# Kernel tuning notes

Measured on AMD Instinct MI355X. Metric: run time of the kernel, lower is better.

## Reference

```python
import jax, jax.numpy as jnp
import numpy as np

SCORE_THRESHOLD = 0.5
IOU_THRESHOLD = 0.5


def _pairwise_iou(boxes):
    # boxes: [N, 4] in xyxy
    x1, y1, x2, y2 = boxes[:, 0], boxes[:, 1], boxes[:, 2], boxes[:, 3]
    area = (x2 - x1) * (y2 - y1)  # [N]
    ix1 = jnp.maximum(x1[:, None], x1[None, :])
    iy1 = jnp.maximum(y1[:, None], y1[None, :])
    ix2 = jnp.minimum(x2[:, None], x2[None, :])
    iy2 = jnp.minimum(y2[:, None], y2[None, :])
    iw = jnp.clip(ix2 - ix1, 0.0)
    ih = jnp.clip(iy2 - iy1, 0.0)
    inter = iw * ih  # [N, N]
    union = area[:, None] + area[None, :] - inter
    return inter / jnp.maximum(union, 1e-9)


def setup_inputs() -> dict:
    key = jax.random.key(0)
    rtdetr_raw_out = jax.random.uniform(key, (1, 8192, 5), dtype=jnp.float32)
    return {"rtdetr_raw_out": rtdetr_raw_out}


def reference(rtdetr_raw_out):
    x = rtdetr_raw_out[0]                      # [N, 5]
    cxcywh = x[:, :4]
    conf = x[:, 4]
    conf = conf / jnp.max(conf)                # normalize by max score
    cx, cy, w, h = cxcywh[:, 0], cxcywh[:, 1], cxcywh[:, 2], cxcywh[:, 3]
    xyxy = jnp.stack([cx - w * 0.5, cy - h * 0.5, cx + w * 0.5, cy + h * 0.5], axis=1)
    valid = conf >= SCORE_THRESHOLD            # score filter
    N = xyxy.shape[0]
    # sort by descending score (torchvision nms processes boxes in score order)
    order = jnp.argsort(-conf)
    boxes_s = xyxy[order]
    scores_s = conf[order]
    valid_s = valid[order]
    iou = _pairwise_iou(boxes_s)               # [N, N]
    idx = jnp.arange(N)

    def body(i, keep):
        # if box i survives, suppress all lower-score boxes with IoU > thr
        sup = keep[i] & (iou[i] > IOU_THRESHOLD) & (idx > i)
        return keep & ~sup

    keep = jax.lax.fori_loop(0, N, body, valid_s)
    out = jnp.concatenate([boxes_s, scores_s[:, None]], axis=1)  # [N, 5]
    # fixed-shape output: suppressed / below-threshold rows are zeroed
    return jnp.where(keep[:, None], out, 0.0)
```

## Files before the change

kernel.cpp:

```cpp
#include <hip/hip_runtime.h>
#include <cstdint>

typedef unsigned long long ull;

#define N_BOX 8192
#define N_WORDS 128
#define CH 512
#define WPC 8
#define NCH 16

#define OFF_TB     0
#define OFF_TD     3932160
#define OFF_BOXES  4456448
#define OFF_SCORES 4587520
#define OFF_RANK   4620288
#define OFF_MASK   4653056
#define OFF_MAXC   4654080
#define OFF_VB     4654084

__device__ __forceinline__ int rows_before(int c) {
    return 8192 * c - 256 * c * (c + 1);
}

__device__ __forceinline__ ull make_key(float s, int idx) {
    return (((ull)__float_as_uint(s)) << 13) | (ull)(8191 - idx);
}

__device__ __forceinline__ float box_area(float4 b) {
    return __fmul_rn(__fsub_rn(b.z, b.x), __fsub_rn(b.w, b.y));
}

__device__ __forceinline__ bool iou_gt_half(float4 a, float aarea, float4 b, float barea) {
    float ix1 = fmaxf(a.x, b.x);
    float iy1 = fmaxf(a.y, b.y);
    float ix2 = fminf(a.z, b.z);
    float iy2 = fminf(a.w, b.w);
    float iw = fmaxf(__fsub_rn(ix2, ix1), 0.0f);
    float ih = fmaxf(__fsub_rn(iy2, iy1), 0.0f);
    float inter = __fmul_rn(iw, ih);
    float uni = __fsub_rn(__fadd_rn(aarea, barea), inter);
    float iou = __fdiv_rn(inter, fmaxf(uni, 1e-9f));
    return iou > 0.5f;
}

__global__ __launch_bounds__(1024) void k1_max_zero(const float* __restrict__ in,
                                                    float* __restrict__ maxc,
                                                    int* __restrict__ rank,
                                                    ull* __restrict__ mask,
                                                    int* __restrict__ vbp) {
    int t = threadIdx.x;
    float m = 0.0f;
    for (int k = t; k < N_BOX; k += 1024) m = fmaxf(m, in[k * 5 + 4]);
    for (int off = 32; off; off >>= 1) m = fmaxf(m, __shfl_down(m, off));
    __shared__ float wm[16];
    if ((t & 63) == 0) wm[t >> 6] = m;
    __syncthreads();
    if (t == 0) {
        float mm = wm[0];
        for (int k = 1; k < 16; ++k) mm = fmaxf(mm, wm[k]);
        *maxc = mm;
        *vbp = 0;
    }
    for (int k = t; k < N_BOX; k += 1024) rank[k] = 0;
    if (t < N_WORDS) mask[t] = 0ull;
}

__global__ __launch_bounds__(256) void k2_rank(const float* __restrict__ in,
                                               const float* __restrict__ maxc_p,
                                               int* __restrict__ rank) {
    __shared__ ull keys[1024];
    int t = threadIdx.x;
    int bx = blockIdx.x;
    int it = bx & 31;
    int jt = bx >> 5;
    float maxc = *maxc_p;
    for (int r = 0; r < 4; ++r) {
        int j = jt * 1024 + r * 256 + t;
        float s = __fdiv_rn(in[j * 5 + 4], maxc);
        keys[r * 256 + t] = make_key(s, j);
    }
    __syncthreads();
    int i = it * 256 + t;
    ull ki = make_key(__fdiv_rn(in[i * 5 + 4], maxc), i);
    int cnt = 0;
    #pragma unroll 8
    for (int k = 0; k < 1024; ++k) cnt += (keys[k] > ki) ? 1 : 0;
    atomicAdd(&rank[i], cnt);
}

__global__ __launch_bounds__(256) void k3_scatter(const float* __restrict__ in,
                                                  const int* __restrict__ rank,
                                                  const float* __restrict__ maxc_p,
                                                  float4* __restrict__ boxes4,
                                                  float* __restrict__ scores,
                                                  ull* __restrict__ mask,
                                                  int* __restrict__ vbp) {
    int i = blockIdx.x * 256 + threadIdx.x;
    float cx = in[i * 5 + 0];
    float cy = in[i * 5 + 1];
    float w  = in[i * 5 + 2];
    float h  = in[i * 5 + 3];
    float c  = in[i * 5 + 4];
    float maxc = *maxc_p;
    float s = __fdiv_rn(c, maxc);
    int r = rank[i];
    float4 b;
    b.x = __fsub_rn(cx, __fmul_rn(w, 0.5f));
    b.y = __fsub_rn(cy, __fmul_rn(h, 0.5f));
    b.z = __fadd_rn(cx, __fmul_rn(w, 0.5f));
    b.w = __fadd_rn(cy, __fmul_rn(h, 0.5f));
    boxes4[r] = b;
    scores[r] = s;
    if (s >= 0.5f) {
        atomicOr(&mask[r >> 6], 1ull << (r & 63));
        atomicAdd(vbp, 1);
    }
}

__global__ __launch_bounds__(256) void k4_build(const float4* __restrict__ boxes4,
                                                const float* __restrict__ scores,
                                                ull* __restrict__ TB,
                                                ull* __restrict__ TD) {
    __shared__ float4 sb[CH];
    __shared__ float sa[CH];
    int bid = blockIdx.x;
    int t = threadIdx.x;
    int c, j0;
    bool diag;
    if (bid >= 1920) {
        diag = true;
        int d = bid - 1920;
        c = d >> 4;
        j0 = (d & 15) * 32;
    } else {
        diag = false;
        c = 0;
        int rem = bid;
        while (rem >= 240 - 16 * c) { rem -= 240 - 16 * c; ++c; }
        j0 = CH * (c + 1) + rem * 32;
    }
    if (scores[c * CH] < 0.5f) return;
    if (!diag && scores[j0] < 0.5f) return;

    for (int i = t; i < CH; i += 256) {
        float4 b = boxes4[c * CH + i];
        sb[i] = b;
        sa[i] = box_area(b);
    }
    __syncthreads();

    int w = t & 7;
    int jj = j0 + (t >> 3);
    if (diag) {
        int jl = jj;
        float4 me = sb[jl];
        float ma = sa[jl];
        int wj = jl >> 6;
        int lim = (w < wj) ? 64 : ((w == wj) ? (jl & 63) : 0);
        ull bits = 0;
        for (int k = 0; k < lim; ++k)
            if (iou_gt_half(sb[w * 64 + k], sa[w * 64 + k], me, ma)) bits |= 1ull << k;
        TD[c * 4096 + w * 512 + jl] = bits;
    } else {
        int j = jj;
        float4 me = boxes4[j];
        float ma = box_area(me);
        ull bits = 0;
        for (int k = 0; k < 64; ++k)
            if (iou_gt_half(sb[w * 64 + k], sa[w * 64 + k], me, ma)) bits |= 1ull << k;
        TB[(size_t)(rows_before(c) + (j - CH * (c + 1))) * WPC + w] = bits;
    }
}

__global__ __launch_bounds__(1024) void k5_nms(const float4* __restrict__ boxes4,
                                               const float* __restrict__ scores,
                                               const ull* __restrict__ gmask,
                                               const ull* __restrict__ TBg,
                                               const ull* __restrict__ TDg,
                                               const int* __restrict__ vbp,
                                               float* __restrict__ out) {
    __shared__ ull TDb[2][CH * WPC];
    __shared__ unsigned amask32[2 * N_WORDS];
    __shared__ ull keptw[WPC];
    __shared__ int svb;
    int t = threadIdx.x;
    int lane = t & 63;
    int wave = t >> 6;

    if (t < 2 * N_WORDS) amask32[t] = ((const unsigned*)gmask)[t];
    if (t == 0) svb = *vbp;
    if (t < WPC) keptw[t] = 0;
    for (int i = t; i < CH * WPC; i += 1024) TDb[0][i] = TDg[i];
    __syncthreads();

    int vb = svb;
    int nchv = (vb + CH - 1) / CH;
    int cur = 0;
    for (int c = 0; c < nchv; ++c) {
        if (wave == 0) {
            const ull* T = TDb[cur];
            ull alive[WPC];
            #pragma unroll
            for (int w = 0; w < WPC; ++w)
                alive[w] = (ull)amask32[c * 16 + 2 * w] |
                           ((ull)amask32[c * 16 + 2 * w + 1] << 32);
            #pragma unroll
            for (int w = 0; w < WPC; ++w) {
                ull word = alive[w];
                if (!word) continue;
                ull td = T[w * 512 + w * 64 + lane];
                ull a2 = word, kept = 0;
                while (a2 & ~kept) {
                    bool al = (a2 >> lane) & 1;
                    bool kp = (kept >> lane) & 1;
                    ull nk = __ballot(al && !kp && ((td & a2) == 0));
                    ull nd = __ballot(al && !kp && ((td & kept) != 0));
                    kept |= nk;
                    a2 &= ~nd;
                }
                alive[w] = kept;
                #pragma unroll
                for (int j = 0; j < WPC; ++j) {
                    if (j <= w) continue;
                    if (!alive[j]) continue;
                    ull m = T[w * 512 + j * 64 + lane];
                    alive[j] &= ~__ballot((m & kept) != 0);
                }
            }
            if (lane == 0) {
                #pragma unroll
                for (int w = 0; w < WPC; ++w) {
                    amask32[c * 16 + 2 * w]     = (unsigned)alive[w];
                    amask32[c * 16 + 2 * w + 1] = (unsigned)(alive[w] >> 32);
                    keptw[w] = alive[w];
                }
            }
        } else if (c + 1 < nchv) {
            int base = (c + 1) * CH * WPC;
            for (int i = t - 64; i < CH * WPC; i += 960) TDb[cur ^ 1][i] = TDg[base + i];
        }
        __syncthreads();

        ull kw[WPC];
        ull anyk = 0;
        #pragma unroll
        for (int k = 0; k < WPC; ++k) { kw[k] = keptw[k]; anyk |= kw[k]; }
        if (anyk) {
            const ull* TBc = TBg + (size_t)rows_before(c) * WPC;
            int jbase = CH * (c + 1);
            for (int j = jbase + t; j < vb; j += 1024) {
                if ((amask32[j >> 5] >> (j & 31)) & 1u) {
                    const ull* r = TBc + (size_t)(j - jbase) * WPC;
                    ull acc = 0;
                    #pragma unroll
                    for (int k = 0; k < WPC; ++k) acc |= r[k] & kw[k];
                    if (acc) atomicAnd(&amask32[j >> 5], ~(1u << (j & 31)));
                }
            }
        }
        cur ^= 1;
        __syncthreads();
    }

    #pragma unroll
    for (int rr = 0; rr < 8; ++rr) {
        int j = t * 8 + rr;
        bool kept = (amask32[j >> 5] >> (j & 31)) & 1u;
        float4 b = boxes4[j];
        float s = scores[j];
        out[j * 5 + 0] = kept ? b.x : 0.0f;
        out[j * 5 + 1] = kept ? b.y : 0.0f;
        out[j * 5 + 2] = kept ? b.z : 0.0f;
        out[j * 5 + 3] = kept ? b.w : 0.0f;
        out[j * 5 + 4] = kept ? s   : 0.0f;
    }
}

extern "C" void kernel_launch(void* const* d_in, const int* in_sizes, int n_in,
                              void* d_out, int out_size, void* d_ws, size_t ws_size,
                              hipStream_t stream) {
    const float* in = (const float*)d_in[0];
    char* ws = (char*)d_ws;
    ull* TB        = (ull*)(ws + OFF_TB);
    ull* TD        = (ull*)(ws + OFF_TD);
    float4* boxes4 = (float4*)(ws + OFF_BOXES);
    float* scores  = (float*)(ws + OFF_SCORES);
    int* rank      = (int*)(ws + OFF_RANK);
    ull* mask      = (ull*)(ws + OFF_MASK);
    float* maxc    = (float*)(ws + OFF_MAXC);
    int* vbp       = (int*)(ws + OFF_VB);
    float* out     = (float*)d_out;

    k1_max_zero<<<1, 1024, 0, stream>>>(in, maxc, rank, mask, vbp);
    k2_rank<<<256, 256, 0, stream>>>(in, maxc, rank);
    k3_scatter<<<32, 256, 0, stream>>>(in, rank, maxc, boxes4, scores, mask, vbp);
    k4_build<<<2176, 256, 0, stream>>>(boxes4, scores, TB, TD);
    k5_nms<<<1, 1024, 0, stream>>>(boxes4, scores, mask, TB, TD, vbp, out);
}
```

Baseline: 144.7 us.

## Overlap deferred far-chunk suppression with next chunk's diagonal resolve in NMS

The single-block NMS kernel now suppresses only the immediately next chunk right after each diagonal resolve. Suppression of the farther chunks is deferred one iteration so waves 1-7 do it while wave 0 resolves the next chunk's diagonal, and waves 8-15 prefetch the next TD tile. The valid mask and count are now derived inside k5 from the sorted scores, since valid boxes form a prefix, which removes atomics from the scatter kernel and zeroing in k1. The diagonal loop also preloads the TD row words into registers. Correctness relies on the deferred suppression finishing before each chunk is used, and on the serial critical path staying the bottleneck.

```diff
diff --git a/kernel.cpp b/kernel.cpp
--- a/kernel.cpp
+++ b/kernel.cpp
@@ -7,16 +7,13 @@
 #define N_WORDS 128
 #define CH 512
 #define WPC 8
-#define NCH 16
 
 #define OFF_TB     0
 #define OFF_TD     3932160
 #define OFF_BOXES  4456448
 #define OFF_SCORES 4587520
 #define OFF_RANK   4620288
-#define OFF_MASK   4653056
-#define OFF_MAXC   4654080
-#define OFF_VB     4654084
+#define OFF_MAXC   4653056
 
 __device__ __forceinline__ int rows_before(int c) {
     return 8192 * c - 256 * c * (c + 1);
@@ -45,9 +42,7 @@
 
 __global__ __launch_bounds__(1024) void k1_max_zero(const float* __restrict__ in,
                                                     float* __restrict__ maxc,
-                                                    int* __restrict__ rank,
-                                                    ull* __restrict__ mask,
-                                                    int* __restrict__ vbp) {
+                                                    int* __restrict__ rank) {
     int t = threadIdx.x;
     float m = 0.0f;
     for (int k = t; k < N_BOX; k += 1024) m = fmaxf(m, in[k * 5 + 4]);
@@ -59,10 +54,8 @@
         float mm = wm[0];
         for (int k = 1; k < 16; ++k) mm = fmaxf(mm, wm[k]);
         *maxc = mm;
-        *vbp = 0;
     }
     for (int k = t; k < N_BOX; k += 1024) rank[k] = 0;
-    if (t < N_WORDS) mask[t] = 0ull;
 }
 
 __global__ __launch_bounds__(256) void k2_rank(const float* __restrict__ in,
@@ -92,9 +85,7 @@
                                                   const int* __restrict__ rank,
                                                   const float* __restrict__ maxc_p,
                                                   float4* __restrict__ boxes4,
-                                                  float* __restrict__ scores,
-                                                  ull* __restrict__ mask,
-                                                  int* __restrict__ vbp) {
+                                                  float* __restrict__ scores) {
     int i = blockIdx.x * 256 + threadIdx.x;
     float cx = in[i * 5 + 0];
     float cy = in[i * 5 + 1];
@@ -111,10 +102,6 @@
     b.w = __fadd_rn(cy, __fmul_rn(h, 0.5f));
     boxes4[r] = b;
     scores[r] = s;
-    if (s >= 0.5f) {
-        atomicOr(&mask[r >> 6], 1ull << (r & 63));
-        atomicAdd(vbp, 1);
-    }
 }
 
 __global__ __launch_bounds__(256) void k4_build(const float4* __restrict__ boxes4,
@@ -174,26 +161,38 @@
 
 __global__ __launch_bounds__(1024) void k5_nms(const float4* __restrict__ boxes4,
                                                const float* __restrict__ scores,
-                                               const ull* __restrict__ gmask,
                                                const ull* __restrict__ TBg,
                                                const ull* __restrict__ TDg,
-                                               const int* __restrict__ vbp,
                                                float* __restrict__ out) {
     __shared__ ull TDb[2][CH * WPC];
     __shared__ unsigned amask32[2 * N_WORDS];
-    __shared__ ull keptw[WPC];
+    __shared__ ull keptA[WPC];
+    __shared__ ull keptB[WPC];
     __shared__ int svb;
     int t = threadIdx.x;
     int lane = t & 63;
     int wave = t >> 6;
 
-    if (t < 2 * N_WORDS) amask32[t] = ((const unsigned*)gmask)[t];
-    if (t == 0) svb = *vbp;
-    if (t < WPC) keptw[t] = 0;
-    for (int i = t; i < CH * WPC; i += 1024) TDb[0][i] = TDg[i];
-    __syncthreads();
-
+    if (t == 0) svb = 0;
+    __syncthreads();
+    {
+        int cnt = 0;
+        #pragma unroll
+        for (int k = 0; k < 8; ++k) cnt += (scores[k * 1024 + t] >= 0.5f) ? 1 : 0;
+        for (int off = 32; off; off >>= 1) cnt += __shfl_down(cnt, off);
+        if (lane == 0) atomicAdd(&svb, cnt);
+    }
+    __syncthreads();
     int vb = svb;
+
+    if (t < 2 * N_WORDS) {
+        int n = vb - t * 32;
+        amask32[t] = (n >= 32) ? 0xffffffffu : ((n <= 0) ? 0u : ((1u << n) - 1u));
+    }
+    if (t < WPC) { keptA[t] = 0; keptB[t] = 0; }
+    for (int i2 = t; i2 < CH * WPC; i2 += 1024) TDb[0][i2] = TDg[i2];
+    __syncthreads();
+
     int nchv = (vb + CH - 1) / CH;
     int cur = 0;
     for (int c = 0; c < nchv; ++c) {
@@ -208,7 +207,11 @@
             for (int w = 0; w < WPC; ++w) {
                 ull word = alive[w];
                 if (!word) continue;
-                ull td = T[w * 512 + w * 64 + lane];
+                ull Tc[WPC];
+                #pragma unroll
+                for (int j = 0; j < WPC; ++j)
+                    if (j >= w) Tc[j] = T[w * 512 + j * 64 + lane];
+                ull td = Tc[w];
                 ull a2 = word, kept = 0;
                 while (a2 & ~kept) {
                     bool al = (a2 >> lane) & 1;
@@ -223,8 +226,7 @@
                 for (int j = 0; j < WPC; ++j) {
                     if (j <= w) continue;
                     if (!alive[j]) continue;
-                    ull m = T[w * 512 + j * 64 + lane];
-                    alive[j] &= ~__ballot((m & kept) != 0);
+                    alive[j] &= ~__ballot((Tc[j] & kept) != 0);
                 }
             }
             if (lane == 0) {
@@ -232,32 +234,61 @@
                 for (int w = 0; w < WPC; ++w) {
                     amask32[c * 16 + 2 * w]     = (unsigned)alive[w];
                     amask32[c * 16 + 2 * w + 1] = (unsigned)(alive[w] >> 32);
-                    keptw[w] = alive[w];
-                }
-            }
-        } else if (c + 1 < nchv) {
-            int base = (c + 1) * CH * WPC;
-            for (int i = t - 64; i < CH * WPC; i += 960) TDb[cur ^ 1][i] = TDg[base + i];
+                    keptA[w] = alive[w];
+                }
+            }
+        } else if (wave < 8) {
+            if (c > 0) {
+                ull kw[WPC];
+                ull anyk = 0;
+                #pragma unroll
+                for (int k = 0; k < WPC; ++k) { kw[k] = keptB[k]; anyk |= kw[k]; }
+                if (anyk) {
+                    const ull* TBc = TBg + (size_t)rows_before(c - 1) * WPC;
+                    int jbase = CH * c;
+                    int jstart = CH * (c + 1);
+                    for (int j = jstart + (t - 64); j < vb; j += 448) {
+                        if ((amask32[j >> 5] >> (j & 31)) & 1u) {
+                            const ull* r = TBc + (size_t)(j - jbase) * WPC;
+                            ull acc = 0;
+                            #pragma unroll
+                            for (int k = 0; k < WPC; ++k) acc |= r[k] & kw[k];
+                            if (acc) atomicAnd(&amask32[j >> 5], ~(1u << (j & 31)));
+                        }
+                    }
+                }
+            }
+        } else {
+            if (c + 1 < nchv) {
+                int base = (c + 1) * CH * WPC;
+                for (int i2 = t - 512; i2 < CH * WPC; i2 += 512)
+                    TDb[cur ^ 1][i2] = TDg[base + i2];
+            }
         }
         __syncthreads();
 
-        ull kw[WPC];
-        ull anyk = 0;
-        #pragma unroll
-        for (int k = 0; k < WPC; ++k) { kw[k] = keptw[k]; anyk |= kw[k]; }
-        if (anyk) {
-            const ull* TBc = TBg + (size_t)rows_before(c) * WPC;
-            int jbase = CH * (c + 1);
-            for (int j = jbase + t; j < vb; j += 1024) {
-                if ((amask32[j >> 5] >> (j & 31)) & 1u) {
-                    const ull* r = TBc + (size_t)(j - jbase) * WPC;
-                    ull acc = 0;
-                    #pragma unroll
-                    for (int k = 0; k < WPC; ++k) acc |= r[k] & kw[k];
-                    if (acc) atomicAnd(&amask32[j >> 5], ~(1u << (j & 31)));
+        if (c + 1 < nchv) {
+            ull kw[WPC];
+            ull anyk = 0;
+            #pragma unroll
+            for (int k = 0; k < WPC; ++k) { kw[k] = keptA[k]; anyk |= kw[k]; }
+            if (anyk) {
+                const ull* TBc = TBg + (size_t)rows_before(c) * WPC;
+                int jbase = CH * (c + 1);
+                int jend = jbase + CH;
+                if (jend > vb) jend = vb;
+                for (int j = jbase + t; j < jend; j += 1024) {
+                    if ((amask32[j >> 5] >> (j & 31)) & 1u) {
+                        const ull* r = TBc + (size_t)(j - jbase) * WPC;
+                        ull acc = 0;
+                        #pragma unroll
+                        for (int k = 0; k < WPC; ++k) acc |= r[k] & kw[k];
+                        if (acc) atomicAnd(&amask32[j >> 5], ~(1u << (j & 31)));
+                    }
                 }
             }
         }
+        if (t < WPC) keptB[t] = keptA[t];
         cur ^= 1;
         __syncthreads();
     }
@@ -286,14 +317,12 @@
     float4* boxes4 = (float4*)(ws + OFF_BOXES);
     float* scores  = (float*)(ws + OFF_SCORES);
     int* rank      = (int*)(ws + OFF_RANK);
-    ull* mask      = (ull*)(ws + OFF_MASK);
     float* maxc    = (float*)(ws + OFF_MAXC);
-    int* vbp       = (int*)(ws + OFF_VB);
     float* out     = (float*)d_out;
 
-    k1_max_zero<<<1, 1024, 0, stream>>>(in, maxc, rank, mask, vbp);
+    k1_max_zero<<<1, 1024, 0, stream>>>(in, maxc, rank);
     k2_rank<<<256, 256, 0, stream>>>(in, maxc, rank);
-    k3_scatter<<<32, 256, 0, stream>>>(in, rank, maxc, boxes4, scores, mask, vbp);
+    k3_scatter<<<32, 256, 0, stream>>>(in, rank, maxc, boxes4, scores);
     k4_build<<<2176, 256, 0, stream>>>(boxes4, scores, TB, TD);
-    k5_nms<<<1, 1024, 0, stream>>>(boxes4, scores, mask, TB, TD, vbp, out);
-}
+    k5_nms<<<1, 1024, 0, stream>>>(boxes4, scores, TB, TD, out);
+}
```

Result: faster. 137.2 us (-5.2%).
